# Kernel tuning notes

Measured on AMD Instinct MI355X. Metric: run time of the kernel, lower is better.

Reference implementation:

```python
import jax, jax.numpy as jnp
import numpy as np

N_NODES = 1000000


def setup_inputs() -> dict:
    key = jax.random.key(0)
    k1, k2, k3 = jax.random.split(key, 3)
    x = jax.random.normal(k1, (N_NODES, 16), dtype=jnp.float32)
    edge_index = jax.random.randint(k2, (2, 4000000), 0, N_NODES, dtype=jnp.int64)
    W = jax.random.normal(k3, (16, 16), dtype=jnp.float32) * (1.0 / np.sqrt(16.0))
    b = jnp.zeros((16,), dtype=jnp.float32)
    return {"x": x, "edge_index": edge_index, "W": W, "b": b}


def reference(x, edge_index, W, b):
    # GCNConv forward: out = D^{-1/2} (A + I) D^{-1/2} (x @ W) + b
    n = x.shape[0]
    row, col = edge_index[0], edge_index[1]  # src, dst

    h = x @ W  # [N, out]

    # degree on target nodes, including self-loops
    deg = jax.ops.segment_sum(jnp.ones_like(col, dtype=h.dtype), col, num_segments=n) + 1.0
    dinv = jax.lax.rsqrt(deg)  # deg >= 1 thanks to self-loops

    # per-edge symmetric normalization, gather-scale-scatter
    norm = dinv[row] * dinv[col]  # [E]
    msgs = h[row] * norm[:, None]  # [E, out]
    agg = jax.ops.segment_sum(msgs, col, num_segments=n)

    # self-loop contribution: norm_ii = dinv[i]^2
    out = agg + h * (dinv * dinv)[:, None] + b
    return out
```

## Files before the change

### kernel.cpp

```cpp
#include <hip/hip_runtime.h>


#define F 16
#define TILE 1024
#define CAP 5120
#define CHUNK 8192
#define CUR_STRIDE 16

static __device__ __forceinline__ unsigned short f2bf(float f) {
    unsigned u = __float_as_uint(f);
    unsigned r = (u + 0x7FFFu + ((u >> 16) & 1u)) >> 16;
    return (unsigned short)r;
}
static __device__ __forceinline__ float bf2f(unsigned short u) {
    return __uint_as_float(((unsigned)u) << 16);
}

__global__ void init_kernel(int* __restrict__ cursor, int nbuck) {
    int b = blockIdx.x * blockDim.x + threadIdx.x;
    if (b < nbuck) cursor[b * CUR_STRIDE] = b * CAP;
}

__global__ void __launch_bounds__(512)
bin_kernel(const int* __restrict__ row, const int* __restrict__ col,
           int* __restrict__ cursor, unsigned* __restrict__ adj, int E, int nbuck) {
    __shared__ int hist[TILE];
    __shared__ int lstart[TILE];
    __shared__ int cnt2[TILE];
    __shared__ int slotBase[TILE];
    __shared__ int scanbuf[512];
    __shared__ unsigned sortedE[CHUNK];
    __shared__ unsigned short sortedBk[CHUNK];

    int t = threadIdx.x;
    for (int i = t; i < TILE; i += 512) { hist[i] = 0; cnt2[i] = 0; }
    __syncthreads();

    int base = blockIdx.x * CHUNK;
    int nE = E - base; if (nE > CHUNK) nE = CHUNK;

    for (int i = t; i < nE; i += 512)
        atomicAdd(&hist[col[base + i] >> 10], 1);
    __syncthreads();

    int a0 = hist[2 * t], a1 = hist[2 * t + 1];
    int s = a0 + a1;
    scanbuf[t] = s;
    __syncthreads();
    for (int off = 1; off < 512; off <<= 1) {
        int y = (t >= off) ? scanbuf[t - off] : 0;
        __syncthreads();
        scanbuf[t] += y;
        __syncthreads();
    }
    int excl = scanbuf[t] - s;
    lstart[2 * t]     = excl;
    lstart[2 * t + 1] = excl + a0;
    if (a0 > 0 && 2 * t < nbuck)
        slotBase[2 * t] = atomicAdd(&cursor[(2 * t) * CUR_STRIDE], a0);
    if (a1 > 0 && 2 * t + 1 < nbuck)
        slotBase[2 * t + 1] = atomicAdd(&cursor[(2 * t + 1) * CUR_STRIDE], a1);
    __syncthreads();

    for (int i = t; i < nE; i += 512) {
        int c = col[base + i];
        int r = row[base + i];
        int bk = c >> 10;
        int li = lstart[bk] + atomicAdd(&cnt2[bk], 1);
        sortedE[li]  = (((unsigned)(c & (TILE - 1))) << 20) | (unsigned)r;
        sortedBk[li] = (unsigned short)bk;
    }
    __syncthreads();

    for (int i = t; i < nE; i += 512) {
        int bk = sortedBk[i];
        int g = slotBase[bk] + (i - lstart[bk]);
        if (g < (bk + 1) * CAP) adj[g] = sortedE[i];
    }
}

__global__ void __launch_bounds__(512)
csr_node_kernel(const int* __restrict__ cursor, unsigned* __restrict__ adj,
                const float* __restrict__ x, const float* __restrict__ W,
                int* __restrict__ ptr, int* __restrict__ deg,
                float* __restrict__ dinv, unsigned short* __restrict__ hs, int N) {
    __shared__ unsigned pk[CAP];
    __shared__ unsigned srt[CAP];
    __shared__ int hist[TILE];
    __shared__ int lstart[TILE];
    __shared__ int cnt2[TILE];
    __shared__ int scanbuf[512];
    __shared__ float sW[256];

    int t = threadIdx.x, b = blockIdx.x;
    if (t < 256) sW[t] = W[t];
    for (int i = t; i < TILE; i += 512) { hist[i] = 0; cnt2[i] = 0; }
    __syncthreads();

    int base = b * CAP;
    int cnt_total = cursor[b * CUR_STRIDE] - base;
    if (cnt_total > CAP) cnt_total = CAP;

    for (int i = t; i < cnt_total; i += 512) {
        unsigned e = adj[base + i];
        pk[i] = e;
        atomicAdd(&hist[e >> 20], 1);
    }
    __syncthreads();

    int a0 = hist[2 * t], a1 = hist[2 * t + 1];
    int s = a0 + a1;
    scanbuf[t] = s;
    __syncthreads();
    for (int off = 1; off < 512; off <<= 1) {
        int y = (t >= off) ? scanbuf[t - off] : 0;
        __syncthreads();
        scanbuf[t] += y;
        __syncthreads();
    }
    int excl = scanbuf[t] - s;
    lstart[2 * t]     = excl;
    lstart[2 * t + 1] = excl + a0;
    {
        int n0 = b * TILE + 2 * t, n1 = n0 + 1;
        if (n0 < N) { ptr[n0] = base + excl;      deg[n0] = a0; dinv[n0] = rsqrtf((float)a0 + 1.0f); }
        if (n1 < N) { ptr[n1] = base + excl + a0; deg[n1] = a1; dinv[n1] = rsqrtf((float)a1 + 1.0f); }
    }
    __syncthreads();

    for (int i = t; i < cnt_total; i += 512) {
        unsigned e = pk[i];
        int cl = e >> 20;
        int pos = lstart[cl] + atomicAdd(&cnt2[cl], 1);
        srt[pos] = e & 0xFFFFFu;
    }
    __syncthreads();
    for (int i = t; i < cnt_total; i += 512)
        adj[base + i] = srt[i];

    #pragma unroll
    for (int p = 0; p < 2; p++) {
        int local = p * 512 + t;
        int node = b * TILE + local;
        if (node >= N) continue;
        float di = rsqrtf((float)hist[local] + 1.0f);

        const float4* xr = (const float4*)(x + (size_t)node * F);
        float4 x0 = xr[0], x1 = xr[1], x2 = xr[2], x3 = xr[3];
        float xv[16] = {x0.x, x0.y, x0.z, x0.w, x1.x, x1.y, x1.z, x1.w,
                        x2.x, x2.y, x2.z, x2.w, x3.x, x3.y, x3.z, x3.w};
        float hv[16];
        #pragma unroll
        for (int j = 0; j < 16; j++) hv[j] = 0.f;
        #pragma unroll
        for (int k = 0; k < 16; k++) {
            float xk = xv[k];
            const float4* wr = (const float4*)(sW + k * 16);
            float4 w0 = wr[0], w1 = wr[1], w2 = wr[2], w3 = wr[3];
            hv[0]  += xk * w0.x; hv[1]  += xk * w0.y; hv[2]  += xk * w0.z; hv[3]  += xk * w0.w;
            hv[4]  += xk * w1.x; hv[5]  += xk * w1.y; hv[6]  += xk * w1.z; hv[7]  += xk * w1.w;
            hv[8]  += xk * w2.x; hv[9]  += xk * w2.y; hv[10] += xk * w2.z; hv[11] += xk * w2.w;
            hv[12] += xk * w3.x; hv[13] += xk * w3.y; hv[14] += xk * w3.z; hv[15] += xk * w3.w;
        }
        unsigned pkk[8];
        #pragma unroll
        for (int q = 0; q < 8; q++)
            pkk[q] = (unsigned)f2bf(hv[2*q] * di) | ((unsigned)f2bf(hv[2*q+1] * di) << 16);
        uint4* hp = (uint4*)(hs + (size_t)node * F);
        hp[0] = make_uint4(pkk[0], pkk[1], pkk[2], pkk[3]);
        hp[1] = make_uint4(pkk[4], pkk[5], pkk[6], pkk[7]);
    }
}

__global__ void __launch_bounds__(256)
gather_kernel(const int* __restrict__ ptr, const int* __restrict__ deg,
              const unsigned* __restrict__ adj, const float* __restrict__ dinv,
              const unsigned short* __restrict__ hs, const float* __restrict__ bias,
              float* __restrict__ out, int N) {
    int tid = blockIdx.x * blockDim.x + threadIdx.x;
    int g = tid >> 4;
    int j = tid & 15;
    if (g >= N) return;

    int p0 = ptr[g];
    int d  = deg[g];
    int end = p0 + d;

    float a0 = bf2f(hs[(size_t)g * F + j]);
    float a1 = 0.f;
    int k = p0;
    for (; k + 1 < end; k += 2) {
        unsigned r0 = adj[k];
        unsigned r1 = adj[k + 1];
        a0 += bf2f(hs[(size_t)r0 * F + j]);
        a1 += bf2f(hs[(size_t)r1 * F + j]);
    }
    if (k < end) a1 += bf2f(hs[(size_t)adj[k] * F + j]);

    out[(size_t)g * F + j] = dinv[g] * (a0 + a1) + bias[j];
}

extern "C" void kernel_launch(void* const* d_in, const int* in_sizes, int n_in,
                              void* d_out, int out_size, void* d_ws, size_t ws_size,
                              hipStream_t stream) {
    const float* x  = (const float*)d_in[0];
    const int*   ei = (const int*)d_in[1];
    const float* W  = (const float*)d_in[2];
    const float* b  = (const float*)d_in[3];

    int N = in_sizes[0] / F;
    int E = in_sizes[1] / 2;
    const int* row = ei;
    const int* col = ei + E;

    float* out = (float*)d_out;
    int nbuck = (N + TILE - 1) / TILE;

    auto align_up = [](size_t v) { return (v + 255) & ~(size_t)255; };
    char* ws = (char*)d_ws;
    size_t off = 0;
    int* cursor = (int*)(ws + off);          off = align_up(off + (size_t)nbuck * CUR_STRIDE * 4);
    unsigned* adj = (unsigned*)(ws + off);   off = align_up(off + (size_t)nbuck * CAP * 4);
    int* ptr  = (int*)(ws + off);            off = align_up(off + (size_t)N * 4);
    int* deg  = (int*)(ws + off);            off = align_up(off + (size_t)N * 4);
    float* dinv = (float*)(ws + off);        off = align_up(off + (size_t)N * 4);
    unsigned short* hs = (unsigned short*)(ws + off); off = align_up(off + (size_t)N * F * 2);

    init_kernel<<<(nbuck + 255) / 256, 256, 0, stream>>>(cursor, nbuck);
    bin_kernel <<<(E + CHUNK - 1) / CHUNK, 512, 0, stream>>>(row, col, cursor, adj, E, nbuck);
    csr_node_kernel<<<nbuck, 512, 0, stream>>>(cursor, adj, x, W, ptr, deg, dinv, hs, N);

    long long gthreads = (long long)N * F;
    gather_kernel<<<(int)((gthreads + 255) / 256), 256, 0, stream>>>
        (ptr, deg, adj, dinv, hs, b, out, N);
}
```

Measured before the change: 318.0 us.

## Use wave-shuffle scans, register-cached edges, packed ptr/deg, and unrolled gather

Replaces the shared-memory Hillis-Steele scans with a wavefront shuffle scan plus per-wave sums, which cuts most block barriers. Edges are held in registers between the histogram and scatter passes instead of being re-read from global or LDS. ptr and deg are packed into one int2, and dinv is recomputed in the gather rather than stored. The gather loads the first 8 neighbours speculatively with nontemporal loads and keeps four accumulators to expose more memory parallelism. The cost is higher register pressure, which may reduce occupancy in the binning kernels.

```diff
diff --git a/kernel.cpp b/kernel.cpp
--- a/kernel.cpp
+++ b/kernel.cpp
@@ -14,6 +14,25 @@
 }
 static __device__ __forceinline__ float bf2f(unsigned short u) {
     return __uint_as_float(((unsigned)u) << 16);
+}
+
+static __device__ __forceinline__ int excl_scan_512(int s, int t, int* wsum) {
+    int lane = t & 63, wv = t >> 6;
+    int incl = s;
+    #pragma unroll
+    for (int off = 1; off < 64; off <<= 1) {
+        int y = __shfl_up(incl, off, 64);
+        if (lane >= off) incl += y;
+    }
+    if (lane == 63) wsum[wv] = incl;
+    __syncthreads();
+    int woff = 0;
+    #pragma unroll
+    for (int w = 0; w < 8; w++) {
+        int v = wsum[w];
+        if (w < wv) woff += v;
+    }
+    return woff + incl - s;
 }
 
 __global__ void init_kernel(int* __restrict__ cursor, int nbuck) {
@@ -28,7 +47,7 @@
     __shared__ int lstart[TILE];
     __shared__ int cnt2[TILE];
     __shared__ int slotBase[TILE];
-    __shared__ int scanbuf[512];
+    __shared__ int wsum[8];
     __shared__ unsigned sortedE[CHUNK];
     __shared__ unsigned short sortedBk[CHUNK];
 
@@ -39,21 +58,23 @@
     int base = blockIdx.x * CHUNK;
     int nE = E - base; if (nE > CHUNK) nE = CHUNK;
 
-    for (int i = t; i < nE; i += 512)
-        atomicAdd(&hist[col[base + i] >> 10], 1);
+    int c[16], r[16];
+    #pragma unroll
+    for (int q = 0; q < 16; q++) {
+        int i = t + q * 512;
+        if (i < nE) {
+            c[q] = col[base + i];
+            r[q] = row[base + i];
+        } else { c[q] = -1; r[q] = 0; }
+    }
+    #pragma unroll
+    for (int q = 0; q < 16; q++)
+        if (c[q] >= 0) atomicAdd(&hist[c[q] >> 10], 1);
     __syncthreads();
 
     int a0 = hist[2 * t], a1 = hist[2 * t + 1];
     int s = a0 + a1;
-    scanbuf[t] = s;
-    __syncthreads();
-    for (int off = 1; off < 512; off <<= 1) {
-        int y = (t >= off) ? scanbuf[t - off] : 0;
-        __syncthreads();
-        scanbuf[t] += y;
-        __syncthreads();
-    }
-    int excl = scanbuf[t] - s;
+    int excl = excl_scan_512(s, t, wsum);
     lstart[2 * t]     = excl;
     lstart[2 * t + 1] = excl + a0;
     if (a0 > 0 && 2 * t < nbuck)
@@ -62,13 +83,14 @@
         slotBase[2 * t + 1] = atomicAdd(&cursor[(2 * t + 1) * CUR_STRIDE], a1);
     __syncthreads();
 
-    for (int i = t; i < nE; i += 512) {
-        int c = col[base + i];
-        int r = row[base + i];
-        int bk = c >> 10;
-        int li = lstart[bk] + atomicAdd(&cnt2[bk], 1);
-        sortedE[li]  = (((unsigned)(c & (TILE - 1))) << 20) | (unsigned)r;
-        sortedBk[li] = (unsigned short)bk;
+    #pragma unroll
+    for (int q = 0; q < 16; q++) {
+        if (c[q] >= 0) {
+            int bk = c[q] >> 10;
+            int li = lstart[bk] + atomicAdd(&cnt2[bk], 1);
+            sortedE[li]  = (((unsigned)(c[q] & (TILE - 1))) << 20) | (unsigned)r[q];
+            sortedBk[li] = (unsigned short)bk;
+        }
     }
     __syncthreads();
 
@@ -82,14 +104,12 @@
 __global__ void __launch_bounds__(512)
 csr_node_kernel(const int* __restrict__ cursor, unsigned* __restrict__ adj,
                 const float* __restrict__ x, const float* __restrict__ W,
-                int* __restrict__ ptr, int* __restrict__ deg,
-                float* __restrict__ dinv, unsigned short* __restrict__ hs, int N) {
-    __shared__ unsigned pk[CAP];
+                int2* __restrict__ pd, unsigned short* __restrict__ hs, int N) {
     __shared__ unsigned srt[CAP];
     __shared__ int hist[TILE];
     __shared__ int lstart[TILE];
     __shared__ int cnt2[TILE];
-    __shared__ int scanbuf[512];
+    __shared__ int wsum[8];
     __shared__ float sW[256];
 
     int t = threadIdx.x, b = blockIdx.x;
@@ -101,42 +121,44 @@
     int cnt_total = cursor[b * CUR_STRIDE] - base;
     if (cnt_total > CAP) cnt_total = CAP;
 
-    for (int i = t; i < cnt_total; i += 512) {
-        unsigned e = adj[base + i];
-        pk[i] = e;
-        atomicAdd(&hist[e >> 20], 1);
+    unsigned e[10];
+    #pragma unroll
+    for (int q = 0; q < 10; q++) {
+        int i = t + q * 512;
+        if (i < cnt_total) {
+            unsigned ee = adj[base + i];
+            e[q] = ee;
+            atomicAdd(&hist[ee >> 20], 1);
+        } else e[q] = 0xFFFFFFFFu;
     }
     __syncthreads();
 
     int a0 = hist[2 * t], a1 = hist[2 * t + 1];
     int s = a0 + a1;
-    scanbuf[t] = s;
-    __syncthreads();
-    for (int off = 1; off < 512; off <<= 1) {
-        int y = (t >= off) ? scanbuf[t - off] : 0;
-        __syncthreads();
-        scanbuf[t] += y;
-        __syncthreads();
-    }
-    int excl = scanbuf[t] - s;
+    int excl = excl_scan_512(s, t, wsum);
     lstart[2 * t]     = excl;
     lstart[2 * t + 1] = excl + a0;
     {
         int n0 = b * TILE + 2 * t, n1 = n0 + 1;
-        if (n0 < N) { ptr[n0] = base + excl;      deg[n0] = a0; dinv[n0] = rsqrtf((float)a0 + 1.0f); }
-        if (n1 < N) { ptr[n1] = base + excl + a0; deg[n1] = a1; dinv[n1] = rsqrtf((float)a1 + 1.0f); }
-    }
-    __syncthreads();
-
-    for (int i = t; i < cnt_total; i += 512) {
-        unsigned e = pk[i];
-        int cl = e >> 20;
-        int pos = lstart[cl] + atomicAdd(&cnt2[cl], 1);
-        srt[pos] = e & 0xFFFFFu;
-    }
-    __syncthreads();
-    for (int i = t; i < cnt_total; i += 512)
-        adj[base + i] = srt[i];
+        if (n0 < N) pd[n0] = make_int2(base + excl,      a0);
+        if (n1 < N) pd[n1] = make_int2(base + excl + a0, a1);
+    }
+    __syncthreads();
+
+    #pragma unroll
+    for (int q = 0; q < 10; q++) {
+        if (e[q] != 0xFFFFFFFFu) {
+            int cl = e[q] >> 20;
+            int pos = lstart[cl] + atomicAdd(&cnt2[cl], 1);
+            srt[pos] = e[q] & 0xFFFFFu;
+        }
+    }
+    __syncthreads();
+    #pragma unroll
+    for (int q = 0; q < 10; q++) {
+        int i = t + q * 512;
+        if (i < cnt_total) adj[base + i] = srt[i];
+    }
 
     #pragma unroll
     for (int p = 0; p < 2; p++) {
@@ -173,8 +195,7 @@
 }
 
 __global__ void __launch_bounds__(256)
-gather_kernel(const int* __restrict__ ptr, const int* __restrict__ deg,
-              const unsigned* __restrict__ adj, const float* __restrict__ dinv,
+gather_kernel(const int2* __restrict__ pd, const unsigned* __restrict__ adj,
               const unsigned short* __restrict__ hs, const float* __restrict__ bias,
               float* __restrict__ out, int N) {
     int tid = blockIdx.x * blockDim.x + threadIdx.x;
@@ -182,22 +203,50 @@
     int j = tid & 15;
     if (g >= N) return;
 
-    int p0 = ptr[g];
-    int d  = deg[g];
-    int end = p0 + d;
-
-    float a0 = bf2f(hs[(size_t)g * F + j]);
-    float a1 = 0.f;
-    int k = p0;
-    for (; k + 1 < end; k += 2) {
-        unsigned r0 = adj[k];
-        unsigned r1 = adj[k + 1];
-        a0 += bf2f(hs[(size_t)r0 * F + j]);
-        a1 += bf2f(hs[(size_t)r1 * F + j]);
-    }
-    if (k < end) a1 += bf2f(hs[(size_t)adj[k] * F + j]);
-
-    out[(size_t)g * F + j] = dinv[g] * (a0 + a1) + bias[j];
+    int2 p = pd[g];
+    int p0 = p.x, d = p.y;
+
+    float s0 = bf2f(hs[(size_t)g * F + j]);
+    float s1 = 0.f, s2 = 0.f, s3 = 0.f;
+
+    unsigned r8[8];
+    #pragma unroll
+    for (int i = 0; i < 8; i++) {
+        unsigned u = __builtin_nontemporal_load(adj + p0 + i);
+        r8[i] = (i < d) ? u : 0u;
+    }
+    float v8[8];
+    #pragma unroll
+    for (int i = 0; i < 8; i++)
+        v8[i] = (i < d) ? bf2f(hs[(size_t)r8[i] * F + j]) : 0.f;
+    s0 += v8[0] + v8[4];
+    s1 += v8[1] + v8[5];
+    s2 += v8[2] + v8[6];
+    s3 += v8[3] + v8[7];
+
+    if (d > 8) {
+        for (int k = 8; k < d; k += 4) {
+            unsigned rr[4];
+            #pragma unroll
+            for (int i = 0; i < 4; i++) {
+                bool ok = (k + i) < d;
+                unsigned u = __builtin_nontemporal_load(adj + p0 + k + (ok ? i : 0));
+                rr[i] = ok ? u : 0u;
+            }
+            #pragma unroll
+            for (int i = 0; i < 4; i++) {
+                float vv = ((k + i) < d) ? bf2f(hs[(size_t)rr[i] * F + j]) : 0.f;
+                if (i == 0) s0 += vv;
+                else if (i == 1) s1 += vv;
+                else if (i == 2) s2 += vv;
+                else s3 += vv;
+            }
+        }
+    }
+
+    float di = rsqrtf((float)d + 1.0f);
+    __builtin_nontemporal_store(di * (s0 + s1 + s2 + s3) + bias[j],
+                                out + (size_t)g * F + j);
 }
 
 extern "C" void kernel_launch(void* const* d_in, const int* in_sizes, int n_in,
@@ -221,16 +270,14 @@
     size_t off = 0;
     int* cursor = (int*)(ws + off);          off = align_up(off + (size_t)nbuck * CUR_STRIDE * 4);
     unsigned* adj = (unsigned*)(ws + off);   off = align_up(off + (size_t)nbuck * CAP * 4);
-    int* ptr  = (int*)(ws + off);            off = align_up(off + (size_t)N * 4);
-    int* deg  = (int*)(ws + off);            off = align_up(off + (size_t)N * 4);
-    float* dinv = (float*)(ws + off);        off = align_up(off + (size_t)N * 4);
+    int2* pd = (int2*)(ws + off);            off = align_up(off + (size_t)N * 8);
     unsigned short* hs = (unsigned short*)(ws + off); off = align_up(off + (size_t)N * F * 2);
 
     init_kernel<<<(nbuck + 255) / 256, 256, 0, stream>>>(cursor, nbuck);
     bin_kernel <<<(E + CHUNK - 1) / CHUNK, 512, 0, stream>>>(row, col, cursor, adj, E, nbuck);
-    csr_node_kernel<<<nbuck, 512, 0, stream>>>(cursor, adj, x, W, ptr, deg, dinv, hs, N);
+    csr_node_kernel<<<nbuck, 512, 0, stream>>>(cursor, adj, x, W, pd, hs, N);
 
     long long gthreads = (long long)N * F;
     gather_kernel<<<(int)((gthreads + 255) / 256), 256, 0, stream>>>
-        (ptr, deg, adj, dinv, hs, b, out, N);
-}
+        (pd, adj, hs, b, out, N);
+}
```

After: 320.4 us. No clear change (+0.8%).
